# Kernel optimization log

Measured on AMD Instinct MI355X. Metric: run time of the kernel, lower is better.

Reference implementation:

```python
import jax, jax.numpy as jnp
import numpy as np
import math

NUM_FREQS = 10
DK = 5
TRADEOFF = 1.0  # euclidean_cosine_tradeoff


def posenc(x, L=NUM_FREQS):
    # NeRF positional encoding without identity: [..., D] -> [..., L*2*D]
    freqs = (2.0 ** jnp.arange(L)).astype(x.dtype)          # [L]
    xb = x[..., None, :] * freqs[:, None]                    # [..., L, D]
    enc = jnp.stack([jnp.sin(xb), jnp.cos(xb)], axis=-2)     # [..., L, 2, D]
    return enc.reshape(x.shape[:-1] + (L * 2 * x.shape[-1],))


def setup_inputs() -> dict:
    key = jax.random.key(0)
    k = jax.random.split(key, 6)
    N, C, E = 500000, 64, 3 * 2 * NUM_FREQS  # 500k points, 64 clusters, embed 60
    X = jax.random.normal(k[0], (N, 3), dtype=jnp.float32)
    cluster_ids = jax.random.randint(k[1], (N,), 0, C)
    linear_mappings = jax.random.normal(k[2], (C * 3, E), dtype=jnp.float32) * 0.1
    # xavier-uniform-like init for Wq/Wk
    lim = math.sqrt(6.0 / (E + DK))
    Wq = jax.random.uniform(k[3], (DK, E), dtype=jnp.float32, minval=-lim, maxval=lim)
    Wk = jax.random.uniform(k[4], (DK, E), dtype=jnp.float32, minval=-lim, maxval=lim)
    Wv = jnp.eye(3, dtype=jnp.float32)  # module sets Wv.weight = eye(3)
    centroids = jax.random.normal(k[5], (C, 3), dtype=jnp.float32)
    return {"X": X, "cluster_ids": cluster_ids, "linear_mappings": linear_mappings,
            "Wq": Wq, "Wk": Wk, "Wv": Wv, "centroids": centroids}


def reference(X, cluster_ids, linear_mappings, Wq, Wk, Wv, centroids):
    N = X.shape[0]
    enc = posenc(X)                                           # [N, 60]
    rgb_clusters = (enc @ linear_mappings.T).reshape(N, -1, 3)  # [N, C, 3]
    # kmeans_rgb = rgb_clusters[arange(N), cluster_ids]
    kmeans_rgb = jnp.take_along_axis(
        rgb_clusters, cluster_ids[:, None, None], axis=1)[:, 0]  # [N, 3]
    # self-attention over clusters
    Q = enc[:, :3 * 2 * NUM_FREQS] @ Wq.T                     # [N, dk]
    K = posenc(centroids) @ Wk.T                              # [C, dk]
    V = rgb_clusters @ Wv.T                                   # [N, C, dv]
    scores = (Q @ K.T) / jnp.asarray(math.sqrt(DK), enc.dtype)  # [N, C]
    attn = jax.nn.softmax(scores, axis=-1)
    # original: per-chunk (attn @ V) then diagonal == per-row weighted sum
    attention_rgb = jnp.einsum('nc,ncd->nd', attn, V)         # [N, 3]
    out = kmeans_rgb * TRADEOFF + attention_rgb * (1.0 - TRADEOFF)
    return out, kmeans_rgb, attention_rgb
```

## Files before the change

### kernel.cpp

```cpp
#include <hip/hip_runtime.h>
#include <math.h>

#define NUM_FREQS 10
#define EDIM 60
#define TRADEOFF 1.0f

typedef __attribute__((ext_vector_type(8))) short bf16x8;
typedef __attribute__((ext_vector_type(4))) float f32x4;

__device__ __forceinline__ short bfc(float f) {
    return __builtin_bit_cast(short, (__bf16)f);
}

__device__ __forceinline__ float swz16(float x) {
    return __builtin_bit_cast(float,
        __builtin_amdgcn_ds_swizzle(__builtin_bit_cast(int, x), 0x401F));
}
__device__ __forceinline__ float sx32(float x) { return __shfl_xor(x, 32, 64); }

__device__ __forceinline__ void posenc3(float x0, float x1, float x2, float* enc) {
    const float inv2pi = 0.15915494309189535f;
    float xs[3] = {x0, x1, x2};
#pragma unroll
    for (int d = 0; d < 3; ++d) {
        float xr = xs[d] * inv2pi;
#pragma unroll
        for (int l = 0; l < NUM_FREQS; ++l) {
            const float fr = __builtin_amdgcn_fractf(xr);
            enc[l*6 + d]     = __builtin_amdgcn_sinf(fr);
            enc[l*6 + 3 + d] = __builtin_amdgcn_cosf(fr);
            xr *= 2.0f;
        }
    }
}

__global__ __launch_bounds__(256) void fused3(
        const float* __restrict__ X,
        const int*   __restrict__ cluster_ids,
        const float* __restrict__ lm,
        const float* __restrict__ Wq,
        const float* __restrict__ Wk,
        const float* __restrict__ Wv,
        const float* __restrict__ cents,
        float* __restrict__ out,
        int N, int nChunks) {
    __shared__ __align__(16) unsigned short sW[256 * 64];
    __shared__ __align__(16) unsigned short sA[256 * 64];
    __shared__ int sCid[256];

    const int tid  = threadIdx.x;
    const int lane = tid & 63;
    const int w    = tid >> 6;
    const int g    = lane >> 4;
    const int l15  = lane & 15;
    const int wbase = w * 64;

    {
        const int r = tid, c = r >> 2, ch = r & 3;
        float row[64];
#pragma unroll
        for (int k = 0; k < 64; ++k) row[k] = 0.f;
        if (ch < 3) {
            const float* src = lm + (3*c + ch) * EDIM;
            for (int k = 0; k < EDIM; ++k) row[k] = src[k];
        } else {
            float enc[EDIM];
            posenc3(cents[c*3+0], cents[c*3+1], cents[c*3+2], enc);
            const float isd = 0.4472135954999579f;
            float kq[5];
#pragma unroll
            for (int j = 0; j < 5; ++j) {
                float a = 0.f;
                for (int k = 0; k < EDIM; ++k) a = fmaf(enc[k], Wk[j*EDIM + k], a);
                kq[j] = a * isd;
            }
            for (int k = 0; k < EDIM; ++k)
                row[k] = Wq[0*EDIM+k]*kq[0] + Wq[1*EDIM+k]*kq[1] + Wq[2*EDIM+k]*kq[2]
                       + Wq[3*EDIM+k]*kq[3] + Wq[4*EDIM+k]*kq[4];
        }
#pragma unroll
        for (int u8 = 0; u8 < 8; ++u8) {
            const int slot = u8 ^ (r & 7);
            bf16x8 v;
#pragma unroll
            for (int j = 0; j < 8; ++j) v[j] = bfc(row[u8*8 + j]);
            *(bf16x8*)&sW[r*64 + slot*8] = v;
        }
    }
    const float wv00 = Wv[0], wv01 = Wv[1], wv02 = Wv[2];
    const float wv10 = Wv[3], wv11 = Wv[4], wv12 = Wv[5];
    const float wv20 = Wv[6], wv21 = Wv[7], wv22 = Wv[8];

    __syncthreads();

    float* o_out = out;
    float* o_km  = out + (size_t)N * 3;
    float* o_at  = out + (size_t)N * 6;

    for (int chunk = blockIdx.x; chunk < nChunks; chunk += gridDim.x) {
        const int base = chunk << 8;

        {
            int n = base + tid; if (n >= N) n = N - 1;
            sCid[tid] = cluster_ids[n];
            float enc[64];
            posenc3(X[n*3+0], X[n*3+1], X[n*3+2], enc);
            enc[60] = 0.f; enc[61] = 0.f; enc[62] = 0.f; enc[63] = 0.f;
#pragma unroll
            for (int u8 = 0; u8 < 8; ++u8) {
                const int slot = u8 ^ (tid & 7);
                bf16x8 v;
#pragma unroll
                for (int j = 0; j < 8; ++j) v[j] = bfc(enc[u8*8 + j]);
                *(bf16x8*)&sA[tid*64 + slot*8] = v;
            }
        }

        for (int h = 0; h < 2; ++h) {
            bf16x8 b0[2], b1[2];
#pragma unroll
            for (int kf = 0; kf < 2; ++kf) {
                const int slot = (kf*4 + g) ^ (l15 & 7);
                b0[kf] = *(const bf16x8*)&sA[(wbase + (2*h  )*16 + l15)*64 + slot*8];
                b1[kf] = *(const bf16x8*)&sA[(wbase + (2*h+1)*16 + l15)*64 + slot*8];
            }
            f32x4 acc0[16], acc1[16];
#pragma unroll
            for (int t = 0; t < 16; ++t) {
                const int row = 16*t + l15;
                const bf16x8 a0 = *(const bf16x8*)&sW[row*64 + (( g   ) ^ (l15 & 7))*8];
                const bf16x8 a1 = *(const bf16x8*)&sW[row*64 + ((4+g) ^ (l15 & 7))*8];
                const f32x4 z = (f32x4){0.f, 0.f, 0.f, 0.f};
                acc0[t] = __builtin_amdgcn_mfma_f32_16x16x32_bf16(a1, b0[1],
                          __builtin_amdgcn_mfma_f32_16x16x32_bf16(a0, b0[0], z, 0,0,0), 0,0,0);
                acc1[t] = __builtin_amdgcn_mfma_f32_16x16x32_bf16(a1, b1[1],
                          __builtin_amdgcn_mfma_f32_16x16x32_bf16(a0, b1[0], z, 0,0,0), 0,0,0);
            }

#pragma unroll
            for (int u = 0; u < 2; ++u) {
                const f32x4* acc = (u == 0) ? acc0 : acc1;
                const int si = 2*h + u;
                const int pl = si*16 + l15;
                const int cid = sCid[wbase + pl];

                float mx = fmaxf(
                    fmaxf(fmaxf(fmaxf(acc[0][3], acc[1][3]), fmaxf(acc[2][3], acc[3][3])),
                          fmaxf(fmaxf(acc[4][3], acc[5][3]), fmaxf(acc[6][3], acc[7][3]))),
                    fmaxf(fmaxf(fmaxf(acc[8][3], acc[9][3]), fmaxf(acc[10][3], acc[11][3])),
                          fmaxf(fmaxf(acc[12][3], acc[13][3]), fmaxf(acc[14][3], acc[15][3]))));
                mx = fmaxf(mx, swz16(mx));
                mx = fmaxf(mx, sx32(mx));

                float S = 0.f, a0s = 0.f, a1s = 0.f, a2s = 0.f;
                float k0 = 0.f, k1 = 0.f, k2 = 0.f;
                const bool gm = ((cid & 3) == g);
                const int  ct = cid >> 2;
#pragma unroll
                for (int t = 0; t < 16; ++t) {
                    const float e = __expf(acc[t][3] - mx);
                    S += e;
                    a0s = fmaf(e, acc[t][0], a0s);
                    a1s = fmaf(e, acc[t][1], a1s);
                    a2s = fmaf(e, acc[t][2], a2s);
                    const bool sel = gm && (ct == t);
                    k0 = sel ? acc[t][0] : k0;
                    k1 = sel ? acc[t][1] : k1;
                    k2 = sel ? acc[t][2] : k2;
                }
                S   += swz16(S);   a0s += swz16(a0s); a1s += swz16(a1s); a2s += swz16(a2s);
                k0  += swz16(k0);  k1  += swz16(k1);  k2  += swz16(k2);
                S   += sx32(S);    a0s += sx32(a0s);  a1s += sx32(a1s);  a2s += sx32(a2s);
                k0  += sx32(k0);   k1  += sx32(k1);   k2  += sx32(k2);

                const int n = base + wbase + pl;
                if (g == 0 && n < N) {
                    const float inv = 1.0f / S;
                    const float u0 = a0s*inv, u1 = a1s*inv, u2 = a2s*inv;
                    const float at0 = wv00*u0 + wv01*u1 + wv02*u2;
                    const float at1 = wv10*u0 + wv11*u1 + wv12*u2;
                    const float at2 = wv20*u0 + wv21*u1 + wv22*u2;
                    const float oo0 = k0*TRADEOFF + at0*(1.0f - TRADEOFF);
                    const float oo1 = k1*TRADEOFF + at1*(1.0f - TRADEOFF);
                    const float oo2 = k2*TRADEOFF + at2*(1.0f - TRADEOFF);
                    o_out[n*3+0] = oo0; o_out[n*3+1] = oo1; o_out[n*3+2] = oo2;
                    o_km[n*3+0]  = k0;  o_km[n*3+1]  = k1;  o_km[n*3+2]  = k2;
                    o_at[n*3+0]  = at0; o_at[n*3+1]  = at1; o_at[n*3+2]  = at2;
                }
            }
        }
    }
}

extern "C" void kernel_launch(void* const* d_in, const int* in_sizes, int n_in,
                              void* d_out, int out_size, void* d_ws, size_t ws_size,
                              hipStream_t stream) {
    const float* X         = (const float*)d_in[0];
    const int*   cids      = (const int*)  d_in[1];
    const float* lm        = (const float*)d_in[2];
    const float* Wq        = (const float*)d_in[3];
    const float* Wk        = (const float*)d_in[4];
    const float* Wv        = (const float*)d_in[5];
    const float* centroids = (const float*)d_in[6];
    float* out = (float*)d_out;
    const int N = in_sizes[0] / 3;

    const int nChunks = (N + 255) / 256;
    const int grid = nChunks < 512 ? nChunks : 512;
    fused3<<<grid, 256, 0, stream>>>(X, cids, lm, Wq, Wk, Wv, centroids, out, N, nChunks);
}
```

Baseline: 124.7 us.

## Build posenc MFMA fragments in registers, drop max-subtraction, raise occupancy

```diff
diff --git a/kernel.cpp b/kernel.cpp
--- a/kernel.cpp
+++ b/kernel.cpp
@@ -8,10 +8,11 @@
 typedef __attribute__((ext_vector_type(8))) short bf16x8;
 typedef __attribute__((ext_vector_type(4))) float f32x4;
 
+#define MFMA(a, b, c) __builtin_amdgcn_mfma_f32_16x16x32_bf16((a), (b), (c), 0, 0, 0)
+
 __device__ __forceinline__ short bfc(float f) {
     return __builtin_bit_cast(short, (__bf16)f);
 }
-
 __device__ __forceinline__ float swz16(float x) {
     return __builtin_bit_cast(float,
         __builtin_amdgcn_ds_swizzle(__builtin_bit_cast(int, x), 0x401F));
@@ -34,7 +35,7 @@
     }
 }
 
-__global__ __launch_bounds__(256) void fused3(
+__global__ __launch_bounds__(256, 4) void fused4(
         const float* __restrict__ X,
         const int*   __restrict__ cluster_ids,
         const float* __restrict__ lm,
@@ -45,46 +46,47 @@
         float* __restrict__ out,
         int N, int nChunks) {
     __shared__ __align__(16) unsigned short sW[256 * 64];
-    __shared__ __align__(16) unsigned short sA[256 * 64];
-    __shared__ int sCid[256];
 
     const int tid  = threadIdx.x;
     const int lane = tid & 63;
     const int w    = tid >> 6;
-    const int g    = lane >> 4;
+    const int g    = (lane >> 4) & 3;
     const int l15  = lane & 15;
-    const int wbase = w * 64;
 
     {
-        const int r = tid, c = r >> 2, ch = r & 3;
-        float row[64];
-#pragma unroll
-        for (int k = 0; k < 64; ++k) row[k] = 0.f;
-        if (ch < 3) {
-            const float* src = lm + (3*c + ch) * EDIM;
-            for (int k = 0; k < EDIM; ++k) row[k] = src[k];
-        } else {
+        const int r = tid, ccl = r >> 2, ch = r & 3;
+        float kq0 = 0.f, kq1 = 0.f, kq2 = 0.f, kq3 = 0.f, kq4 = 0.f;
+        if (ch == 3) {
             float enc[EDIM];
-            posenc3(cents[c*3+0], cents[c*3+1], cents[c*3+2], enc);
+            posenc3(cents[ccl*3+0], cents[ccl*3+1], cents[ccl*3+2], enc);
             const float isd = 0.4472135954999579f;
-            float kq[5];
+            float kk[5];
 #pragma unroll
             for (int j = 0; j < 5; ++j) {
                 float a = 0.f;
                 for (int k = 0; k < EDIM; ++k) a = fmaf(enc[k], Wk[j*EDIM + k], a);
-                kq[j] = a * isd;
-            }
-            for (int k = 0; k < EDIM; ++k)
-                row[k] = Wq[0*EDIM+k]*kq[0] + Wq[1*EDIM+k]*kq[1] + Wq[2*EDIM+k]*kq[2]
-                       + Wq[3*EDIM+k]*kq[3] + Wq[4*EDIM+k]*kq[4];
-        }
-#pragma unroll
-        for (int u8 = 0; u8 < 8; ++u8) {
-            const int slot = u8 ^ (r & 7);
+                kk[j] = a * isd;
+            }
+            kq0 = kk[0]; kq1 = kk[1]; kq2 = kk[2]; kq3 = kk[3]; kq4 = kk[4];
+        }
+        const float* lrow = lm + (3*ccl + (ch < 3 ? ch : 0)) * EDIM;
+#pragma unroll
+        for (int b = 0; b < 8; ++b) {
             bf16x8 v;
 #pragma unroll
-            for (int j = 0; j < 8; ++j) v[j] = bfc(row[u8*8 + j]);
-            *(bf16x8*)&sW[r*64 + slot*8] = v;
+            for (int j = 0; j < 8; ++j) {
+                const int p = b*4 + (j >> 1), cc = j & 1;
+                float val = 0.f;
+                if (p < 30) {
+                    const int l = (p*11) >> 5, d = p - 3*l;
+                    const int sig = 6*l + 3*cc + d;
+                    if (ch < 3) val = lrow[sig];
+                    else val = Wq[sig]*kq0 + Wq[60+sig]*kq1 + Wq[120+sig]*kq2
+                             + Wq[180+sig]*kq3 + Wq[240+sig]*kq4;
+                }
+                v[j] = bfc(val);
+            }
+            *(bf16x8*)&sW[r*64 + (b ^ (r & 7))*8] = v;
         }
     }
     const float wv00 = Wv[0], wv01 = Wv[1], wv02 = Wv[2];
@@ -97,96 +99,124 @@
     float* o_km  = out + (size_t)N * 3;
     float* o_at  = out + (size_t)N * 6;
 
+    const float inv2pi = 0.15915494309189535f;
+    const int slot0 = (g ^ (l15 & 7)) * 8;
+    const int slot1 = ((4 + g) ^ (l15 & 7)) * 8;
+
     for (int chunk = blockIdx.x; chunk < nChunks; chunk += gridDim.x) {
-        const int base = chunk << 8;
-
-        {
-            int n = base + tid; if (n >= N) n = N - 1;
-            sCid[tid] = cluster_ids[n];
-            float enc[64];
-            posenc3(X[n*3+0], X[n*3+1], X[n*3+2], enc);
-            enc[60] = 0.f; enc[61] = 0.f; enc[62] = 0.f; enc[63] = 0.f;
-#pragma unroll
-            for (int u8 = 0; u8 < 8; ++u8) {
-                const int slot = u8 ^ (tid & 7);
-                bf16x8 v;
-#pragma unroll
-                for (int j = 0; j < 8; ++j) v[j] = bfc(enc[u8*8 + j]);
-                *(bf16x8*)&sA[tid*64 + slot*8] = v;
-            }
-        }
-
+        const int base = (chunk << 8) + w*64;
+
+#pragma unroll
         for (int h = 0; h < 2; ++h) {
-            bf16x8 b0[2], b1[2];
-#pragma unroll
-            for (int kf = 0; kf < 2; ++kf) {
-                const int slot = (kf*4 + g) ^ (l15 & 7);
-                b0[kf] = *(const bf16x8*)&sA[(wbase + (2*h  )*16 + l15)*64 + slot*8];
-                b1[kf] = *(const bf16x8*)&sA[(wbase + (2*h+1)*16 + l15)*64 + slot*8];
-            }
-            f32x4 acc0[16], acc1[16];
-#pragma unroll
-            for (int t = 0; t < 16; ++t) {
-                const int row = 16*t + l15;
-                const bf16x8 a0 = *(const bf16x8*)&sW[row*64 + (( g   ) ^ (l15 & 7))*8];
-                const bf16x8 a1 = *(const bf16x8*)&sW[row*64 + ((4+g) ^ (l15 & 7))*8];
-                const f32x4 z = (f32x4){0.f, 0.f, 0.f, 0.f};
-                acc0[t] = __builtin_amdgcn_mfma_f32_16x16x32_bf16(a1, b0[1],
-                          __builtin_amdgcn_mfma_f32_16x16x32_bf16(a0, b0[0], z, 0,0,0), 0,0,0);
-                acc1[t] = __builtin_amdgcn_mfma_f32_16x16x32_bf16(a1, b1[1],
-                          __builtin_amdgcn_mfma_f32_16x16x32_bf16(a0, b1[0], z, 0,0,0), 0,0,0);
-            }
-
+            bf16x8 bfr[2][2];
+            int cid0, cid1, n0, n1;
 #pragma unroll
             for (int u = 0; u < 2; ++u) {
-                const f32x4* acc = (u == 0) ? acc0 : acc1;
-                const int si = 2*h + u;
-                const int pl = si*16 + l15;
-                const int cid = sCid[wbase + pl];
-
-                float mx = fmaxf(
-                    fmaxf(fmaxf(fmaxf(acc[0][3], acc[1][3]), fmaxf(acc[2][3], acc[3][3])),
-                          fmaxf(fmaxf(acc[4][3], acc[5][3]), fmaxf(acc[6][3], acc[7][3]))),
-                    fmaxf(fmaxf(fmaxf(acc[8][3], acc[9][3]), fmaxf(acc[10][3], acc[11][3])),
-                          fmaxf(fmaxf(acc[12][3], acc[13][3]), fmaxf(acc[14][3], acc[15][3]))));
-                mx = fmaxf(mx, swz16(mx));
-                mx = fmaxf(mx, sx32(mx));
-
-                float S = 0.f, a0s = 0.f, a1s = 0.f, a2s = 0.f;
-                float k0 = 0.f, k1 = 0.f, k2 = 0.f;
-                const bool gm = ((cid & 3) == g);
-                const int  ct = cid >> 2;
-#pragma unroll
-                for (int t = 0; t < 16; ++t) {
-                    const float e = __expf(acc[t][3] - mx);
-                    S += e;
-                    a0s = fmaf(e, acc[t][0], a0s);
-                    a1s = fmaf(e, acc[t][1], a1s);
-                    a2s = fmaf(e, acc[t][2], a2s);
-                    const bool sel = gm && (ct == t);
-                    k0 = sel ? acc[t][0] : k0;
-                    k1 = sel ? acc[t][1] : k1;
-                    k2 = sel ? acc[t][2] : k2;
-                }
-                S   += swz16(S);   a0s += swz16(a0s); a1s += swz16(a1s); a2s += swz16(a2s);
-                k0  += swz16(k0);  k1  += swz16(k1);  k2  += swz16(k2);
-                S   += sx32(S);    a0s += sx32(a0s);  a1s += sx32(a1s);  a2s += sx32(a2s);
-                k0  += sx32(k0);   k1  += sx32(k1);   k2  += sx32(k2);
-
-                const int n = base + wbase + pl;
-                if (g == 0 && n < N) {
-                    const float inv = 1.0f / S;
-                    const float u0 = a0s*inv, u1 = a1s*inv, u2 = a2s*inv;
-                    const float at0 = wv00*u0 + wv01*u1 + wv02*u2;
-                    const float at1 = wv10*u0 + wv11*u1 + wv12*u2;
-                    const float at2 = wv20*u0 + wv21*u1 + wv22*u2;
-                    const float oo0 = k0*TRADEOFF + at0*(1.0f - TRADEOFF);
-                    const float oo1 = k1*TRADEOFF + at1*(1.0f - TRADEOFF);
-                    const float oo2 = k2*TRADEOFF + at2*(1.0f - TRADEOFF);
-                    o_out[n*3+0] = oo0; o_out[n*3+1] = oo1; o_out[n*3+2] = oo2;
-                    o_km[n*3+0]  = k0;  o_km[n*3+1]  = k1;  o_km[n*3+2]  = k2;
-                    o_at[n*3+0]  = at0; o_at[n*3+1]  = at1; o_at[n*3+2]  = at2;
-                }
+                const int n = base + (2*h + u)*16 + l15;
+                const int nc = n < N ? n : N - 1;
+                if (u == 0) { n0 = n; cid0 = cluster_ids[nc]; }
+                else        { n1 = n; cid1 = cluster_ids[nc]; }
+                const float r0 = X[nc*3+0] * inv2pi;
+                const float r1 = X[nc*3+1] * inv2pi;
+                const float r2 = X[nc*3+2] * inv2pi;
+#pragma unroll
+                for (int kf = 0; kf < 2; ++kf) {
+                    const int b = kf*4 + g;
+                    bf16x8 v;
+#pragma unroll
+                    for (int i = 0; i < 4; ++i) {
+                        const int p = b*4 + i;
+                        const int l = (p*11) >> 5;
+                        const int d = p - 3*l;
+                        const float rd = (d == 0) ? r0 : ((d == 1) ? r1 : r2);
+                        const float t  = ldexpf(rd, l);
+                        const float fr = __builtin_amdgcn_fractf(t);
+                        const float sv = __builtin_amdgcn_sinf(fr);
+                        const float cv = __builtin_amdgcn_cosf(fr);
+                        const bool ok = (p < 30);
+                        v[2*i]   = ok ? bfc(sv) : (short)0;
+                        v[2*i+1] = ok ? bfc(cv) : (short)0;
+                    }
+                    bfr[u][kf] = v;
+                }
+            }
+
+            float S0=0.f, A00=0.f, A10=0.f, A20=0.f, K00=0.f, K10=0.f, K20=0.f;
+            float S1=0.f, A01=0.f, A11=0.f, A21=0.f, K01=0.f, K11=0.f, K21=0.f;
+
+#pragma unroll
+            for (int half = 0; half < 2; ++half) {
+                f32x4 acc[2][8];
+#pragma unroll
+                for (int t = 0; t < 8; ++t) {
+                    const int row = (half*8 + t)*16 + l15;
+                    const bf16x8 a0 = *(const bf16x8*)&sW[row*64 + slot0];
+                    const bf16x8 a1 = *(const bf16x8*)&sW[row*64 + slot1];
+                    const f32x4 z = (f32x4){0.f, 0.f, 0.f, 0.f};
+                    acc[0][t] = MFMA(a1, bfr[0][1], MFMA(a0, bfr[0][0], z));
+                    acc[1][t] = MFMA(a1, bfr[1][1], MFMA(a0, bfr[1][0], z));
+                }
+#pragma unroll
+                for (int t = 0; t < 8; ++t) {
+                    const int cl = 4*(half*8 + t) + g;
+                    {
+                        const float e = __expf(acc[0][t][3]);
+                        S0 += e;
+                        A00 = fmaf(e, acc[0][t][0], A00);
+                        A10 = fmaf(e, acc[0][t][1], A10);
+                        A20 = fmaf(e, acc[0][t][2], A20);
+                        const bool sel = (cid0 == cl);
+                        K00 = sel ? acc[0][t][0] : K00;
+                        K10 = sel ? acc[0][t][1] : K10;
+                        K20 = sel ? acc[0][t][2] : K20;
+                    }
+                    {
+                        const float e = __expf(acc[1][t][3]);
+                        S1 += e;
+                        A01 = fmaf(e, acc[1][t][0], A01);
+                        A11 = fmaf(e, acc[1][t][1], A11);
+                        A21 = fmaf(e, acc[1][t][2], A21);
+                        const bool sel = (cid1 == cl);
+                        K01 = sel ? acc[1][t][0] : K01;
+                        K11 = sel ? acc[1][t][1] : K11;
+                        K21 = sel ? acc[1][t][2] : K21;
+                    }
+                }
+            }
+
+            S0 += swz16(S0); A00 += swz16(A00); A10 += swz16(A10); A20 += swz16(A20);
+            K00 += swz16(K00); K10 += swz16(K10); K20 += swz16(K20);
+            S0 += sx32(S0);  A00 += sx32(A00);  A10 += sx32(A10);  A20 += sx32(A20);
+            K00 += sx32(K00); K10 += sx32(K10); K20 += sx32(K20);
+
+            S1 += swz16(S1); A01 += swz16(A01); A11 += swz16(A11); A21 += swz16(A21);
+            K01 += swz16(K01); K11 += swz16(K11); K21 += swz16(K21);
+            S1 += sx32(S1);  A01 += sx32(A01);  A11 += sx32(A11);  A21 += sx32(A21);
+            K01 += sx32(K01); K11 += sx32(K11); K21 += sx32(K21);
+
+            if (g == 0 && n0 < N) {
+                const float inv = 1.0f / S0;
+                const float u0 = A00*inv, u1 = A10*inv, u2 = A20*inv;
+                const float at0 = wv00*u0 + wv01*u1 + wv02*u2;
+                const float at1 = wv10*u0 + wv11*u1 + wv12*u2;
+                const float at2 = wv20*u0 + wv21*u1 + wv22*u2;
+                o_out[n0*3+0] = K00*TRADEOFF + at0*(1.0f - TRADEOFF);
+                o_out[n0*3+1] = K10*TRADEOFF + at1*(1.0f - TRADEOFF);
+                o_out[n0*3+2] = K20*TRADEOFF + at2*(1.0f - TRADEOFF);
+                o_km[n0*3+0] = K00; o_km[n0*3+1] = K10; o_km[n0*3+2] = K20;
+                o_at[n0*3+0] = at0; o_at[n0*3+1] = at1; o_at[n0*3+2] = at2;
+            }
+            if (g == 0 && n1 < N) {
+                const float inv = 1.0f / S1;
+                const float u0 = A01*inv, u1 = A11*inv, u2 = A21*inv;
+                const float at0 = wv00*u0 + wv01*u1 + wv02*u2;
+                const float at1 = wv10*u0 + wv11*u1 + wv12*u2;
+                const float at2 = wv20*u0 + wv21*u1 + wv22*u2;
+                o_out[n1*3+0] = K01*TRADEOFF + at0*(1.0f - TRADEOFF);
+                o_out[n1*3+1] = K11*TRADEOFF + at1*(1.0f - TRADEOFF);
+                o_out[n1*3+2] = K21*TRADEOFF + at2*(1.0f - TRADEOFF);
+                o_km[n1*3+0] = K01; o_km[n1*3+1] = K11; o_km[n1*3+2] = K21;
+                o_at[n1*3+0] = at0; o_at[n1*3+1] = at1; o_at[n1*3+2] = at2;
             }
         }
     }
@@ -206,6 +236,6 @@
     const int N = in_sizes[0] / 3;
 
     const int nChunks = (N + 255) / 256;
-    const int grid = nChunks < 512 ? nChunks : 512;
-    fused3<<<grid, 256, 0, stream>>>(X, cids, lm, Wq, Wk, Wv, centroids, out, N, nChunks);
-}
+    const int grid = nChunks < 1024 ? nChunks : 1024;
+    fused4<<<grid, 256, 0, stream>>>(X, cids, lm, Wq, Wk, Wv, centroids, out, N, nChunks);
+}
```

Measured after the change: 177.3 us. 42.2% more time.
